# Kernel optimization log

Measured on AMD Instinct MI355X. Metric: run time of the kernel, lower is better.

Reference implementation:

```python
import jax, jax.numpy as jnp
import numpy as np

B, S, D, H = 4, 2048, 512, 8
DH = D // H


def setup_inputs() -> dict:
    key = jax.random.key(0)
    ks = jax.random.split(key, 6)
    embeddings = jax.random.normal(ks[0], (B, S, D), dtype=jnp.float32)
    token_masks = jax.random.randint(ks[1], (B, S), 0, 2, dtype=jnp.int32)
    # keras 'random_normal' initializer: stddev 0.05
    Wq = 0.05 * jax.random.normal(ks[2], (D, D), dtype=jnp.float32)
    Wk = 0.05 * jax.random.normal(ks[3], (D, D), dtype=jnp.float32)
    Wv = 0.05 * jax.random.normal(ks[4], (D, D), dtype=jnp.float32)
    Wo = 0.05 * jax.random.normal(ks[5], (D, D), dtype=jnp.float32)
    return {"embeddings": embeddings, "token_masks": token_masks,
            "Wq": Wq, "Wk": Wk, "Wv": Wv, "Wo": Wo}


def reference(embeddings, token_masks, Wq, Wk, Wv, Wo):
    b, s, d = embeddings.shape
    h, dh = H, d // H
    # QKV projections -> (b, h, s, dh)
    def split_heads(x):
        return x.reshape(b, s, h, dh).transpose(0, 2, 1, 3)
    Q = split_heads(embeddings @ Wq)
    K = split_heads(embeddings @ Wk)
    V = split_heads(embeddings @ Wv)
    scores = jnp.einsum('bhqd,bhkd->bhqk', Q, K) / jnp.sqrt(jnp.float32(dh))
    # causal (lower-triangular) mask combined with padding mask on both q and k
    causal = jnp.tril(jnp.ones((s, s), dtype=jnp.float32))
    tm = token_masks.astype(jnp.float32)
    attn_mask = causal[None, None, :, :] * tm[:, None, None, :] * tm[:, None, :, None]
    scores = jnp.where(attn_mask > 0, scores, jnp.float32(-1e30))
    weights = jax.nn.softmax(scores, axis=-1)  # dropout omitted (inference/eval mode)
    context = jnp.einsum('bhqk,bhkd->bhqd', weights, V)
    context = context.transpose(0, 2, 1, 3).reshape(b, s, d)
    return context @ Wo
```

## Files before the change

### kernel.cpp

```cpp
#include <hip/hip_runtime.h>
#include <hip/hip_bf16.h>
#include <stdint.h>

#define BATCH 4
#define SEQ 2048
#define DMODEL 512
#define NHEAD 8
#define HD 64

#define C1 0.18033688f
#define BIAS2 -23.0831207f

using f32x4 = __attribute__((ext_vector_type(4))) float;
using bfrag = __attribute__((ext_vector_type(8))) short;

__device__ __forceinline__ short f2bf(float f) {
  uint32_t x = __builtin_bit_cast(uint32_t, f);
  uint32_t r = (x + 0x7fffu + ((x >> 16) & 1u)) >> 16;
  return (short)r;
}
__device__ __forceinline__ short f2bf_fast(float f) {
  return (short)((__builtin_bit_cast(uint32_t, f) + 0x8000u) >> 16);
}
__device__ __forceinline__ float bf2f(short s) {
  return __builtin_bit_cast(float, ((uint32_t)(uint16_t)s) << 16);
}
__device__ __forceinline__ void gl_lds16(const void* g, void* l) {
  __builtin_amdgcn_global_load_lds(
      (const __attribute__((address_space(1))) void*)g,
      (__attribute__((address_space(3))) void*)l, 16, 0, 0);
}
__device__ __forceinline__ bool sniff_f32(const void* p, int tid) {
  const uint32_t* xw = (const uint32_t*)p;
  const int lane = tid & 63;
  const uint32_t w1 = xw[lane], w2 = xw[64 + lane];
  bool bad = (((w1 >> 7) & 0xffu) >= 0xB0u) | (((w1 >> 23) & 0xffu) >= 0xB0u) |
             (((w2 >> 7) & 0xffu) >= 0xB0u) | (((w2 >> 23) & 0xffu) >= 0xB0u);
  return __ballot(bad) != 0ull;
}

__global__ __launch_bounds__(256) void prep(const void* __restrict__ X,
                                            const void* __restrict__ w0,
                                            const void* __restrict__ w1,
                                            const void* __restrict__ w2,
                                            const void* __restrict__ w3,
                                            short* __restrict__ Xb,
                                            short* __restrict__ wtAll,
                                            float* __restrict__ mv) {
  const int blk = blockIdx.x, tid = threadIdx.x;
  if (blk < 2048) {
    const bool isf32 = sniff_f32(X, tid);
    const int i = (blk * 256 + tid) * 8;
    if (isf32) {
      const float* f = (const float*)X;
      short r[8];
#pragma unroll
      for (int j = 0; j < 8; ++j) r[j] = f2bf(f[i + j]);
      *(bfrag*)&Xb[i] = *(bfrag*)r;
    } else {
      *(bfrag*)&Xb[i] = *(const bfrag*)&((const short*)X)[i];
    }
  } else if (blk < 3072) {
    __shared__ short t[32][33];
    const int idx = blk - 2048;
    const int z = idx >> 8, rem = idx & 255;
    const void* in = (z == 0) ? w0 : (z == 1) ? w1 : (z == 2) ? w2 : w3;
    short* out = wtAll + (size_t)z * DMODEL * DMODEL;
    const int tx = tid & 31, ty = tid >> 5;
    const bool isf32 = sniff_f32(in, tid);
    const int n0 = (rem & 15) * 32, k0 = (rem >> 4) * 32;
#pragma unroll
    for (int i = ty; i < 32; i += 8) {
      const int idx2 = (k0 + i) * DMODEL + n0 + tx;
      t[i][tx] = isf32 ? f2bf(((const float*)in)[idx2]) : ((const short*)in)[idx2];
    }
    __syncthreads();
#pragma unroll
    for (int i = ty; i < 32; i += 8) out[(n0 + i) * DMODEL + k0 + tx] = t[tx][i];
  } else {
#pragma unroll
    for (int j = 0; j < 8; ++j) mv[tid * 8 + j] = 0.f;
  }
}

__global__ __launch_bounds__(256) void gemm_qkv(const short* __restrict__ X,
                                                const short* __restrict__ WtAll,
                                                short* __restrict__ Qo,
                                                short* __restrict__ Ko,
                                                short* __restrict__ Vo,
                                                float* __restrict__ mv) {
  __shared__ __align__(16) short As[128 * 32];
  __shared__ __align__(16) short Bs[128 * 32];
  const int which = blockIdx.z;
  const short* Wt = WtAll + which * DMODEL * DMODEL;
  const int m0 = blockIdx.y * 128, n0 = blockIdx.x * 128;
  const int tid = threadIdx.x, lane = tid & 63, wave = tid >> 6;
  const int l15 = lane & 15, quad = lane >> 4;
  const int wm = wave >> 1, wn = wave & 1;
  const int lrow = lane >> 2, lcol = (lane & 3) * 8;
  f32x4 acc[4][4] = {};
  for (int kc = 0; kc < DMODEL; kc += 32) {
#pragma unroll
    for (int i = 0; i < 2; ++i) {
      const int r0 = (wave * 2 + i) * 16;
      gl_lds16(&X[(size_t)(m0 + r0 + lrow) * DMODEL + kc + lcol], &As[r0 * 32]);
      gl_lds16(&Wt[(size_t)(n0 + r0 + lrow) * DMODEL + kc + lcol], &Bs[r0 * 32]);
    }
    __syncthreads();
    bfrag a[4], b[4];
#pragma unroll
    for (int t = 0; t < 4; ++t) {
      a[t] = *(const bfrag*)&As[(wm * 64 + t * 16 + l15) * 32 + quad * 8];
      b[t] = *(const bfrag*)&Bs[(wn * 64 + t * 16 + l15) * 32 + quad * 8];
    }
#pragma unroll
    for (int tm = 0; tm < 4; ++tm)
#pragma unroll
      for (int tn = 0; tn < 4; ++tn)
        acc[tm][tn] = __builtin_amdgcn_mfma_f32_16x16x32_bf16(a[tm], b[tn], acc[tm][tn], 0, 0, 0);
    __syncthreads();
  }
  short* O = (which == 0) ? Qo : (which == 1) ? Ko : Vo;
#pragma unroll
  for (int tn = 0; tn < 4; ++tn) {
    const int col = n0 + wn * 64 + tn * 16 + l15;
    const int h = col >> 6, d = col & 63;
#pragma unroll
    for (int tm = 0; tm < 4; ++tm) {
#pragma unroll
      for (int r = 0; r < 4; ++r) {
        const int row = m0 + wm * 64 + tm * 16 + quad * 4 + r;
        const int b = row >> 11, s = row & 2047;
        O[((b * NHEAD + h) * SEQ + s) * HD + d] = f2bf(acc[tm][tn][r]);
      }
    }
  }
  if (which == 2) {
    const int b = (m0 + wm * 64) >> 11;
#pragma unroll
    for (int tn = 0; tn < 4; ++tn) {
      float s = 0.f;
#pragma unroll
      for (int tm = 0; tm < 4; ++tm)
#pragma unroll
        for (int r = 0; r < 4; ++r) s += acc[tm][tn][r];
      s += __shfl_xor(s, 16);
      s += __shfl_xor(s, 32);
      if (quad == 0) {
        const int col = n0 + wn * 64 + tn * 16 + l15;
        const int h = col >> 6, d = col & 63;
        atomicAdd(&mv[(b * NHEAD + h) * 64 + d], s);
      }
    }
  }
}

__global__ __launch_bounds__(256) void gemm_out(const short* __restrict__ X,
                                                const short* __restrict__ Wt,
                                                float* __restrict__ O) {
  __shared__ __align__(16) short As[128 * 32];
  __shared__ __align__(16) short Bs[128 * 32];
  const int m0 = blockIdx.y * 128, n0 = blockIdx.x * 128;
  const int tid = threadIdx.x, lane = tid & 63, wave = tid >> 6;
  const int l15 = lane & 15, quad = lane >> 4;
  const int wm = wave >> 1, wn = wave & 1;
  const int lrow = lane >> 2, lcol = (lane & 3) * 8;
  f32x4 acc[4][4] = {};
  for (int kc = 0; kc < DMODEL; kc += 32) {
#pragma unroll
    for (int i = 0; i < 2; ++i) {
      const int r0 = (wave * 2 + i) * 16;
      gl_lds16(&X[(size_t)(m0 + r0 + lrow) * DMODEL + kc + lcol], &As[r0 * 32]);
      gl_lds16(&Wt[(size_t)(n0 + r0 + lrow) * DMODEL + kc + lcol], &Bs[r0 * 32]);
    }
    __syncthreads();
    bfrag a[4], b[4];
#pragma unroll
    for (int t = 0; t < 4; ++t) {
      a[t] = *(const bfrag*)&As[(wm * 64 + t * 16 + l15) * 32 + quad * 8];
      b[t] = *(const bfrag*)&Bs[(wn * 64 + t * 16 + l15) * 32 + quad * 8];
    }
#pragma unroll
    for (int tm = 0; tm < 4; ++tm)
#pragma unroll
      for (int tn = 0; tn < 4; ++tn)
        acc[tm][tn] = __builtin_amdgcn_mfma_f32_16x16x32_bf16(a[tm], b[tn], acc[tm][tn], 0, 0, 0);
    __syncthreads();
  }
#pragma unroll
  for (int tm = 0; tm < 4; ++tm)
#pragma unroll
    for (int tn = 0; tn < 4; ++tn) {
      const int col = n0 + wn * 64 + tn * 16 + l15;
#pragma unroll
      for (int r = 0; r < 4; ++r) {
        const int row = m0 + wm * 64 + tm * 16 + quad * 4 + r;
        O[(size_t)row * DMODEL + col] = acc[tm][tn][r];
      }
    }
}

__global__ __launch_bounds__(256, 4) void attn(const short* __restrict__ Q,
                                               const short* __restrict__ K,
                                               const short* __restrict__ V,
                                               const int* __restrict__ tmask,
                                               const float* __restrict__ meanV,
                                               short* __restrict__ ctx) {
  __shared__ __align__(16) short Ks[64 * 72];
  __shared__ __align__(16) short Vts[64 * 64];
  __shared__ __align__(16) short Ps[4 * 16 * 64];
  __shared__ int tmq[64];
  __shared__ int tmk[64];
  const int m2 = blockIdx.x >> 3, a3 = blockIdx.x & 7;
  const int j2 = blockIdx.y >> 3, b3 = blockIdx.y & 7;
  const int quart = (m2 + j2) & 3;
  const int qi = quart * 8 + ((quart & 1) ? (7 - a3) : a3);
  const int bh = j2 * 8 + b3;
  const int b = bh >> 3, h = bh & 7;
  const int q0 = qi * 64;
  const int tid = threadIdx.x, lane = tid & 63, wave = tid >> 6;
  const int l15 = lane & 15, quad = lane >> 4;
  const size_t base = (size_t)bh * SEQ * HD;

  bfrag qa0 = *(const bfrag*)&Q[base + (size_t)(q0 + wave * 16 + l15) * HD + quad * 8];
  bfrag qa1 = *(const bfrag*)&Q[base + (size_t)(q0 + wave * 16 + l15) * HD + 32 + quad * 8];
  if (tid < 64) tmq[tid] = tmask[b * SEQ + q0 + tid];

  f32x4 accO[4] = {};
  float lrow[4] = {0.f, 0.f, 0.f, 0.f};

  const int rp = tid >> 3, sgp = tid & 7;
  bfrag kA, kB, vA, vB;
  int tmreg = 0;

  auto prefetch = [&](int kc) {
    const size_t o0 = base + (size_t)(kc + 2 * rp) * HD + sgp * 8;
    kA = *(const bfrag*)&K[o0];
    kB = *(const bfrag*)&K[o0 + HD];
    vA = *(const bfrag*)&V[o0];
    vB = *(const bfrag*)&V[o0 + HD];
    if (tid < 64) tmreg = tmask[b * SEQ + kc + tid];
  };
  auto store_lds = [&]() {
    *(bfrag*)&Ks[(2 * rp) * 72 + sgp * 8] = kA;
    *(bfrag*)&Ks[(2 * rp + 1) * 72 + sgp * 8] = kB;
    const int g = ((rp >> 2) ^ sgp) & 7;
    const int kpos = (2 * rp) & 7;
#pragma unroll
    for (int j = 0; j < 8; ++j) {
      const uint32_t w = (uint32_t)(uint16_t)vA[j] | ((uint32_t)(uint16_t)vB[j] << 16);
      *(uint32_t*)&Vts[(sgp * 8 + j) * 64 + g * 8 + kpos] = w;
    }
    if (tid < 64) tmk[tid] = tmreg;
  };
  auto compute = [&](bool diag) {
    f32x4 sacc[4] = {};
#pragma unroll
    for (int t = 0; t < 4; ++t) {
      bfrag b0 = *(const bfrag*)&Ks[(t * 16 + l15) * 72 + quad * 8];
      sacc[t] = __builtin_amdgcn_mfma_f32_16x16x32_bf16(qa0, b0, sacc[t], 0, 0, 0);
    }
#pragma unroll
    for (int t = 0; t < 4; ++t) {
      bfrag b1 = *(const bfrag*)&Ks[(t * 16 + l15) * 72 + 32 + quad * 8];
      sacc[t] = __builtin_amdgcn_mfma_f32_16x16x32_bf16(qa1, b1, sacc[t], 0, 0, 0);
    }
    float badd[4];
#pragma unroll
    for (int t = 0; t < 4; ++t) badd[t] = tmk[t * 16 + l15] ? BIAS2 : -1e30f;
#pragma unroll
    for (int r = 0; r < 4; ++r) {
      const int m = quad * 4 + r;
#pragma unroll
      for (int t = 0; t < 4; ++t) {
        float p = exp2f(fmaf(sacc[t][r], C1, badd[t]));
        if (diag && (t * 16 + l15 > wave * 16 + m)) p = 0.f;
        lrow[r] += p;
        const int g = ((t * 2 + (l15 >> 3)) ^ (m & 7) ^ ((m >> 3) << 1)) & 7;
        Ps[wave * 1024 + m * 64 + g * 8 + (l15 & 7)] = f2bf_fast(p);
      }
    }
#pragma unroll
    for (int ks = 0; ks < 2; ++ks) {
#pragma unroll
      for (int t = 0; t < 4; ++t) {
        const int gp = ((ks * 4 + quad) ^ (l15 & 7) ^ ((l15 >> 3) << 1)) & 7;
        bfrag pa = *(const bfrag*)&Ps[wave * 1024 + l15 * 64 + gp * 8];
        const int d = t * 16 + l15;
        const int gv = ((ks * 4 + quad) ^ (d >> 3)) & 7;
        bfrag vb = *(const bfrag*)&Vts[d * 64 + gv * 8];
        accO[t] = __builtin_amdgcn_mfma_f32_16x16x32_bf16(pa, vb, accO[t], 0, 0, 0);
      }
    }
  };

  prefetch(0);
  for (int kc = 0; kc <= q0; kc += 64) {
    __syncthreads();
    store_lds();
    __syncthreads();
    if (kc < q0) prefetch(kc + 64);
    compute(kc == q0);
  }

#pragma unroll
  for (int r = 0; r < 4; ++r) {
    float l = lrow[r];
    l += __shfl_xor(l, 1);
    l += __shfl_xor(l, 2);
    l += __shfl_xor(l, 4);
    l += __shfl_xor(l, 8);
    lrow[r] = 1.f / l;
  }
  const int qrow_loc = wave * 16 + quad * 4;
#pragma unroll
  for (int t = 0; t < 4; ++t) {
    const int d = t * 16 + l15;
    const float mvd = meanV[bh * 64 + d] * (1.f / 2048.f);
#pragma unroll
    for (int r = 0; r < 4; ++r) {
      const int row = qrow_loc + r;
      float val = accO[t][r] * lrow[r];
      if (tmq[row] == 0) val = mvd;
      ctx[((size_t)(b * SEQ + q0 + row)) * DMODEL + h * HD + d] = f2bf(val);
    }
  }
}

extern "C" void kernel_launch(void* const* d_in, const int* in_sizes, int n_in,
                              void* d_out, int out_size, void* d_ws, size_t ws_size,
                              hipStream_t stream) {
  const void* X = d_in[0];
  const int* tmask = (const int*)d_in[1];
  const void* Wq = d_in[2];
  const void* Wk = d_in[3];
  const void* Wv = d_in[4];
  const void* Wo = d_in[5];
  float* out = (float*)d_out;
  char* ws = (char*)d_ws;

  const size_t WELEM = (size_t)DMODEL * DMODEL;
  const size_t TELEM = (size_t)BATCH * NHEAD * SEQ * HD;

  float* mv = (float*)(ws + 4096);
  short* wt = (short*)(ws + 4096 + 8192);
  short* Xb = (short*)(ws + 4096 + 8192 + 2097152);
  short* Qb = Xb + TELEM;
  short* Kb = Qb + TELEM;
  short* Vb = Kb + TELEM;
  short* Cb = Vb + TELEM;

  prep<<<3073, 256, 0, stream>>>(X, Wq, Wk, Wv, Wo, Xb, wt, mv);
  gemm_qkv<<<dim3(4, 64, 3), 256, 0, stream>>>(Xb, wt, Qb, Kb, Vb, mv);
  attn<<<dim3(32, 32), 256, 0, stream>>>(Qb, Kb, Vb, tmask, mv, Cb);
  gemm_out<<<dim3(4, 64), 256, 0, stream>>>(Cb, wt + 3 * WELEM, out);
}
```

Before: 180.7 us.

## Shrink GEMM tiles and read K fragments directly from global in attention

```diff
diff --git a/kernel.cpp b/kernel.cpp
--- a/kernel.cpp
+++ b/kernel.cpp
@@ -90,41 +90,44 @@
                                                 short* __restrict__ Vo,
                                                 float* __restrict__ mv) {
   __shared__ __align__(16) short As[128 * 32];
-  __shared__ __align__(16) short Bs[128 * 32];
+  __shared__ __align__(16) short Bs[64 * 32];
   const int which = blockIdx.z;
   const short* Wt = WtAll + which * DMODEL * DMODEL;
-  const int m0 = blockIdx.y * 128, n0 = blockIdx.x * 128;
+  const int m0 = blockIdx.y * 128, n0 = blockIdx.x * 64;
   const int tid = threadIdx.x, lane = tid & 63, wave = tid >> 6;
   const int l15 = lane & 15, quad = lane >> 4;
   const int wm = wave >> 1, wn = wave & 1;
   const int lrow = lane >> 2, lcol = (lane & 3) * 8;
-  f32x4 acc[4][4] = {};
+  f32x4 acc[4][2] = {};
   for (int kc = 0; kc < DMODEL; kc += 32) {
 #pragma unroll
     for (int i = 0; i < 2; ++i) {
-      const int r0 = (wave * 2 + i) * 16;
+      const int r0 = wave * 32 + i * 16;
       gl_lds16(&X[(size_t)(m0 + r0 + lrow) * DMODEL + kc + lcol], &As[r0 * 32]);
-      gl_lds16(&Wt[(size_t)(n0 + r0 + lrow) * DMODEL + kc + lcol], &Bs[r0 * 32]);
-    }
-    __syncthreads();
-    bfrag a[4], b[4];
-#pragma unroll
-    for (int t = 0; t < 4; ++t) {
+    }
+    gl_lds16(&Wt[(size_t)(n0 + wave * 16 + lrow) * DMODEL + kc + lcol],
+             &Bs[wave * 16 * 32]);
+    __syncthreads();
+    bfrag a[4], b[2];
+#pragma unroll
+    for (int t = 0; t < 4; ++t)
       a[t] = *(const bfrag*)&As[(wm * 64 + t * 16 + l15) * 32 + quad * 8];
-      b[t] = *(const bfrag*)&Bs[(wn * 64 + t * 16 + l15) * 32 + quad * 8];
-    }
+#pragma unroll
+    for (int t = 0; t < 2; ++t)
+      b[t] = *(const bfrag*)&Bs[(wn * 32 + t * 16 + l15) * 32 + quad * 8];
 #pragma unroll
     for (int tm = 0; tm < 4; ++tm)
 #pragma unroll
-      for (int tn = 0; tn < 4; ++tn)
+      for (int tn = 0; tn < 2; ++tn)
         acc[tm][tn] = __builtin_amdgcn_mfma_f32_16x16x32_bf16(a[tm], b[tn], acc[tm][tn], 0, 0, 0);
     __syncthreads();
   }
   short* O = (which == 0) ? Qo : (which == 1) ? Ko : Vo;
-#pragma unroll
-  for (int tn = 0; tn < 4; ++tn) {
-    const int col = n0 + wn * 64 + tn * 16 + l15;
-    const int h = col >> 6, d = col & 63;
+  const int h = n0 >> 6;
+#pragma unroll
+  for (int tn = 0; tn < 2; ++tn) {
+    const int col = n0 + wn * 32 + tn * 16 + l15;
+    const int d = col & 63;
 #pragma unroll
     for (int tm = 0; tm < 4; ++tm) {
 #pragma unroll
@@ -136,9 +139,9 @@
     }
   }
   if (which == 2) {
-    const int b = (m0 + wm * 64) >> 11;
-#pragma unroll
-    for (int tn = 0; tn < 4; ++tn) {
+    const int b = m0 >> 11;
+#pragma unroll
+    for (int tn = 0; tn < 2; ++tn) {
       float s = 0.f;
 #pragma unroll
       for (int tm = 0; tm < 4; ++tm)
@@ -147,9 +150,8 @@
       s += __shfl_xor(s, 16);
       s += __shfl_xor(s, 32);
       if (quad == 0) {
-        const int col = n0 + wn * 64 + tn * 16 + l15;
-        const int h = col >> 6, d = col & 63;
-        atomicAdd(&mv[(b * NHEAD + h) * 64 + d], s);
+        const int col = n0 + wn * 32 + tn * 16 + l15;
+        atomicAdd(&mv[(b * NHEAD + h) * 64 + (col & 63)], s);
       }
     }
   }
@@ -158,46 +160,36 @@
 __global__ __launch_bounds__(256) void gemm_out(const short* __restrict__ X,
                                                 const short* __restrict__ Wt,
                                                 float* __restrict__ O) {
-  __shared__ __align__(16) short As[128 * 32];
-  __shared__ __align__(16) short Bs[128 * 32];
-  const int m0 = blockIdx.y * 128, n0 = blockIdx.x * 128;
+  __shared__ __align__(16) short As[64 * 32];
+  __shared__ __align__(16) short Bs[64 * 32];
+  const int m0 = blockIdx.y * 64, n0 = blockIdx.x * 64;
   const int tid = threadIdx.x, lane = tid & 63, wave = tid >> 6;
   const int l15 = lane & 15, quad = lane >> 4;
-  const int wm = wave >> 1, wn = wave & 1;
   const int lrow = lane >> 2, lcol = (lane & 3) * 8;
-  f32x4 acc[4][4] = {};
+  f32x4 acc[4] = {};
   for (int kc = 0; kc < DMODEL; kc += 32) {
-#pragma unroll
-    for (int i = 0; i < 2; ++i) {
-      const int r0 = (wave * 2 + i) * 16;
-      gl_lds16(&X[(size_t)(m0 + r0 + lrow) * DMODEL + kc + lcol], &As[r0 * 32]);
-      gl_lds16(&Wt[(size_t)(n0 + r0 + lrow) * DMODEL + kc + lcol], &Bs[r0 * 32]);
-    }
-    __syncthreads();
-    bfrag a[4], b[4];
+    gl_lds16(&X[(size_t)(m0 + wave * 16 + lrow) * DMODEL + kc + lcol],
+             &As[wave * 16 * 32]);
+    gl_lds16(&Wt[(size_t)(n0 + wave * 16 + lrow) * DMODEL + kc + lcol],
+             &Bs[wave * 16 * 32]);
+    __syncthreads();
+    bfrag a = *(const bfrag*)&As[(wave * 16 + l15) * 32 + quad * 8];
 #pragma unroll
     for (int t = 0; t < 4; ++t) {
-      a[t] = *(const bfrag*)&As[(wm * 64 + t * 16 + l15) * 32 + quad * 8];
-      b[t] = *(const bfrag*)&Bs[(wn * 64 + t * 16 + l15) * 32 + quad * 8];
-    }
-#pragma unroll
-    for (int tm = 0; tm < 4; ++tm)
-#pragma unroll
-      for (int tn = 0; tn < 4; ++tn)
-        acc[tm][tn] = __builtin_amdgcn_mfma_f32_16x16x32_bf16(a[tm], b[tn], acc[tm][tn], 0, 0, 0);
-    __syncthreads();
-  }
-#pragma unroll
-  for (int tm = 0; tm < 4; ++tm)
-#pragma unroll
-    for (int tn = 0; tn < 4; ++tn) {
-      const int col = n0 + wn * 64 + tn * 16 + l15;
-#pragma unroll
-      for (int r = 0; r < 4; ++r) {
-        const int row = m0 + wm * 64 + tm * 16 + quad * 4 + r;
-        O[(size_t)row * DMODEL + col] = acc[tm][tn][r];
-      }
-    }
+      bfrag b = *(const bfrag*)&Bs[(t * 16 + l15) * 32 + quad * 8];
+      acc[t] = __builtin_amdgcn_mfma_f32_16x16x32_bf16(a, b, acc[t], 0, 0, 0);
+    }
+    __syncthreads();
+  }
+#pragma unroll
+  for (int t = 0; t < 4; ++t) {
+    const int col = n0 + t * 16 + l15;
+#pragma unroll
+    for (int r = 0; r < 4; ++r) {
+      const int row = m0 + wave * 16 + quad * 4 + r;
+      O[(size_t)row * DMODEL + col] = acc[t][r];
+    }
+  }
 }
 
 __global__ __launch_bounds__(256, 4) void attn(const short* __restrict__ Q,
@@ -206,7 +198,6 @@
                                                const int* __restrict__ tmask,
                                                const float* __restrict__ meanV,
                                                short* __restrict__ ctx) {
-  __shared__ __align__(16) short Ks[64 * 72];
   __shared__ __align__(16) short Vts[64 * 64];
   __shared__ __align__(16) short Ps[4 * 16 * 64];
   __shared__ int tmq[64];
@@ -230,20 +221,16 @@
   float lrow[4] = {0.f, 0.f, 0.f, 0.f};
 
   const int rp = tid >> 3, sgp = tid & 7;
-  bfrag kA, kB, vA, vB;
+  bfrag vA, vB;
   int tmreg = 0;
 
   auto prefetch = [&](int kc) {
     const size_t o0 = base + (size_t)(kc + 2 * rp) * HD + sgp * 8;
-    kA = *(const bfrag*)&K[o0];
-    kB = *(const bfrag*)&K[o0 + HD];
     vA = *(const bfrag*)&V[o0];
     vB = *(const bfrag*)&V[o0 + HD];
     if (tid < 64) tmreg = tmask[b * SEQ + kc + tid];
   };
   auto store_lds = [&]() {
-    *(bfrag*)&Ks[(2 * rp) * 72 + sgp * 8] = kA;
-    *(bfrag*)&Ks[(2 * rp + 1) * 72 + sgp * 8] = kB;
     const int g = ((rp >> 2) ^ sgp) & 7;
     const int kpos = (2 * rp) & 7;
 #pragma unroll
@@ -253,16 +240,17 @@
     }
     if (tid < 64) tmk[tid] = tmreg;
   };
-  auto compute = [&](bool diag) {
+  auto compute = [&](int kc, bool diag) {
+    const short* Kc = &K[base + (size_t)kc * HD];
     f32x4 sacc[4] = {};
 #pragma unroll
     for (int t = 0; t < 4; ++t) {
-      bfrag b0 = *(const bfrag*)&Ks[(t * 16 + l15) * 72 + quad * 8];
+      bfrag b0 = *(const bfrag*)&Kc[(t * 16 + l15) * HD + quad * 8];
       sacc[t] = __builtin_amdgcn_mfma_f32_16x16x32_bf16(qa0, b0, sacc[t], 0, 0, 0);
     }
 #pragma unroll
     for (int t = 0; t < 4; ++t) {
-      bfrag b1 = *(const bfrag*)&Ks[(t * 16 + l15) * 72 + 32 + quad * 8];
+      bfrag b1 = *(const bfrag*)&Kc[(t * 16 + l15) * HD + 32 + quad * 8];
       sacc[t] = __builtin_amdgcn_mfma_f32_16x16x32_bf16(qa1, b1, sacc[t], 0, 0, 0);
     }
     float badd[4];
@@ -282,10 +270,10 @@
     }
 #pragma unroll
     for (int ks = 0; ks < 2; ++ks) {
+      const int gp = ((ks * 4 + quad) ^ (l15 & 7) ^ ((l15 >> 3) << 1)) & 7;
+      bfrag pa = *(const bfrag*)&Ps[wave * 1024 + l15 * 64 + gp * 8];
 #pragma unroll
       for (int t = 0; t < 4; ++t) {
-        const int gp = ((ks * 4 + quad) ^ (l15 & 7) ^ ((l15 >> 3) << 1)) & 7;
-        bfrag pa = *(const bfrag*)&Ps[wave * 1024 + l15 * 64 + gp * 8];
         const int d = t * 16 + l15;
         const int gv = ((ks * 4 + quad) ^ (d >> 3)) & 7;
         bfrag vb = *(const bfrag*)&Vts[d * 64 + gv * 8];
@@ -300,7 +288,7 @@
     store_lds();
     __syncthreads();
     if (kc < q0) prefetch(kc + 64);
-    compute(kc == q0);
+    compute(kc, kc == q0);
   }
 
 #pragma unroll
@@ -351,7 +339,7 @@
   short* Cb = Vb + TELEM;
 
   prep<<<3073, 256, 0, stream>>>(X, Wq, Wk, Wv, Wo, Xb, wt, mv);
-  gemm_qkv<<<dim3(4, 64, 3), 256, 0, stream>>>(Xb, wt, Qb, Kb, Vb, mv);
+  gemm_qkv<<<dim3(8, 64, 3), 256, 0, stream>>>(Xb, wt, Qb, Kb, Vb, mv);
   attn<<<dim3(32, 32), 256, 0, stream>>>(Qb, Kb, Vb, tmask, mv, Cb);
-  gemm_out<<<dim3(4, 64), 256, 0, stream>>>(Cb, wt + 3 * WELEM, out);
-}
+  gemm_out<<<dim3(8, 128), 256, 0, stream>>>(Cb, wt + 3 * WELEM, out);
+}
```

After: 215.2 us. 19.1% more time.
